# Performance work log

Measured on AMD Instinct MI355X. Metric: run time of the kernel, lower is better.

## Reference

```python
import jax, jax.numpy as jnp
import numpy as np

N_NODES = 100000
N_EDGES = 1600000
HIDDEN = 64
IN_CH = 6  # 3 (direction) + 3 (node feature part)
BN_EPS = 1e-5


def setup_inputs() -> dict:
    key = jax.random.key(0)
    ks = jax.random.split(key, 16)
    inp = {
        "x": jax.random.normal(ks[0], (N_NODES, 3), dtype=jnp.float32),
        "pos": jax.random.normal(ks[1], (N_NODES, 3), dtype=jnp.float32),
        "edge_index": jax.random.randint(ks[2], (2, N_EDGES), 0, N_NODES, dtype=jnp.int64),
    }
    dims = [IN_CH, HIDDEN, HIDDEN, HIDDEN]
    for i in range(3):
        din, dout = dims[i], dims[i + 1]
        inp[f"W{i+1}"] = jax.random.normal(ks[3 + 4 * i], (din, dout), dtype=jnp.float32) * (1.0 / np.sqrt(din))
        inp[f"b{i+1}"] = jnp.zeros((dout,), dtype=jnp.float32)
        inp[f"g{i+1}"] = jnp.ones((dout,), dtype=jnp.float32)   # BN gamma
        inp[f"be{i+1}"] = jnp.zeros((dout,), dtype=jnp.float32)  # BN beta
    return inp


def _mlp_layer(h, W, b, g, be):
    # Linear -> ReLU -> BatchNorm1d (training mode, biased variance like torch)
    h = jax.nn.relu(h @ W + b)
    mu = jnp.mean(h, axis=0)
    var = jnp.mean((h - mu) ** 2, axis=0)
    return g * (h - mu) * jax.lax.rsqrt(var + BN_EPS) + be


def reference(x, pos, edge_index, W1, b1, g1, be1, W2, b2, g2, be2, W3, b3, g3, be3):
    n = x.shape[0]
    xp = jnp.concatenate([pos, x], axis=1)             # [N, 3+F]
    src, dst = edge_index[0], edge_index[1]            # j = src, i = dst (PyG source_to_target)
    x_j = xp[src]                                      # [E, 3+F]
    x_i = xp[dst]
    direction = x_j[:, :3] - x_i[:, :3]                # [E, 3]
    # NOTE: source uses torch.norm with no dim => single global scalar norm
    direction = direction / jnp.linalg.norm(direction)
    h = jnp.concatenate([direction, x_i[:, 3:]], axis=-1)  # [E, IN_CH]
    h = _mlp_layer(h, W1, b1, g1, be1)
    h = _mlp_layer(h, W2, b2, g2, be2)
    h = _mlp_layer(h, W3, b3, g3, be3)                 # [E, HIDDEN]
    out = jax.ops.segment_max(h, dst, num_segments=n)  # scatter-max aggregation
    out = jnp.where(jnp.isfinite(out), out, 0.0)       # PyG fills empty segments with 0
    return out
```

## Files before the change

### kernel.cpp

```cpp
#include <hip/hip_runtime.h>
#include <stdint.h>

typedef unsigned short u16;
typedef unsigned int u32;
typedef __attribute__((ext_vector_type(8))) short short8;
typedef __attribute__((ext_vector_type(4))) float floatx4;

#define BN_EPS 1e-5f
#define NPB 64
#define NPB_SHIFT 6
#define NBMAX 2048

__device__ __forceinline__ float bf2f(u16 u) { return __uint_as_float(((unsigned)u) << 16); }
__device__ __forceinline__ u16 f2bf(float f) {
  unsigned u = __float_as_uint(f);
  u += 0x7FFFu + ((u >> 16) & 1u);
  return (u16)(u >> 16);
}
__device__ __forceinline__ u32 fkey(float f) {
  unsigned u = __float_as_uint(f);
  return (u >> 31) ? ~u : (u | 0x80000000u);
}
__device__ __forceinline__ float funkey(u32 k) {
  return (k & 0x80000000u) ? __uint_as_float(k ^ 0x80000000u) : __uint_as_float(~k);
}

__global__ void k_init(float* __restrict__ stats, u32* __restrict__ bucketTotal) {
  for (int i = threadIdx.x; i < 1024; i += blockDim.x) stats[i] = 0.f;
  for (int i = threadIdx.x; i < NBMAX + 1; i += blockDim.x) bucketTotal[i] = 0u;
}

__global__ void k_norm_hist(const int* __restrict__ ei, const float* __restrict__ pos,
                            int E, int NB, float* __restrict__ stats,
                            u32* __restrict__ bucketTotal) {
  __shared__ u32 lh[NBMAX];
  __shared__ float red[16];
  for (int i = threadIdx.x; i < NB; i += blockDim.x) lh[i] = 0u;
  __syncthreads();
  int tid = blockIdx.x * blockDim.x + threadIdx.x;
  int stride = gridDim.x * blockDim.x;
  float acc = 0.f;
  for (int e = tid; e < E; e += stride) {
    int s = ei[e], d = ei[E + e];
    float d0 = pos[3 * s + 0] - pos[3 * d + 0];
    float d1 = pos[3 * s + 1] - pos[3 * d + 1];
    float d2 = pos[3 * s + 2] - pos[3 * d + 2];
    acc = fmaf(d0, d0, acc);
    acc = fmaf(d1, d1, acc);
    acc = fmaf(d2, d2, acc);
    atomicAdd(&lh[d >> NPB_SHIFT], 1u);
  }
#pragma unroll
  for (int off = 32; off > 0; off >>= 1) acc += __shfl_down(acc, off, 64);
  if ((threadIdx.x & 63) == 0) red[threadIdx.x >> 6] = acc;
  __syncthreads();
  if (threadIdx.x == 0) {
    float s = 0.f;
    for (int w = 0; w < (int)(blockDim.x >> 6); w++) s += red[w];
    atomicAdd(&stats[0], s);
  }
  for (int i = threadIdx.x; i < NB; i += blockDim.x)
    if (lh[i]) atomicAdd(&bucketTotal[i], lh[i]);
}

__global__ void k_scan(const u32* __restrict__ bucketTotal, u32* __restrict__ base,
                       u32* __restrict__ cursor, int NB) {
  int lane = threadIdx.x;
  u32 run = 0;
  for (int b0 = 0; b0 < NB; b0 += 64) {
    int b = b0 + lane;
    u32 v = (b < NB) ? bucketTotal[b] : 0u;
    u32 s = v;
#pragma unroll
    for (int off = 1; off < 64; off <<= 1) {
      u32 t = __shfl_up(s, off, 64);
      if (lane >= off) s += t;
    }
    u32 excl = run + s - v;
    if (b < NB) { base[b] = excl; cursor[b] = excl; }
    run += __shfl(s, 63, 64);
  }
  if (lane == 0) base[NB] = run;
}

__global__ void k_place(const int* __restrict__ ei, int E, int NB,
                        u32* __restrict__ cursor, u32* __restrict__ sorted) {
  __shared__ u32 lh[NBMAX];
  __shared__ u32 lbase[NBMAX];
  for (int i = threadIdx.x; i < NB; i += blockDim.x) lh[i] = 0u;
  __syncthreads();
  int tid = blockIdx.x * blockDim.x + threadIdx.x;
  int stride = gridDim.x * blockDim.x;
  for (int e = tid; e < E; e += stride) atomicAdd(&lh[ei[E + e] >> NPB_SHIFT], 1u);
  __syncthreads();
  for (int i = threadIdx.x; i < NB; i += blockDim.x) {
    u32 c = lh[i];
    lbase[i] = c ? atomicAdd(&cursor[i], c) : 0u;
    lh[i] = 0u;
  }
  __syncthreads();
  for (int e = tid; e < E; e += stride) {
    int d = ei[E + e];
    int b = d >> NPB_SHIFT;
    u32 slot = lbase[b] + atomicAdd(&lh[b], 1u);
    sorted[slot] = ((u32)e << 8) | (u32)(d & (NPB - 1));
  }
}

__global__ __launch_bounds__(256) void k_bucket_max(
    const u32* __restrict__ sorted, const u32* __restrict__ base,
    const u16* __restrict__ h, const float* __restrict__ gsum3,
    const float* __restrict__ gsq3, const float* __restrict__ g3,
    const float* __restrict__ be3, float invE, float* __restrict__ outf, int N) {
  __shared__ u32 tile[NPB * 64];
  for (int i = threadIdx.x; i < NPB * 64; i += blockDim.x) tile[i] = 0u;
  int b = blockIdx.x;
  u32 start = base[b];
  int cnt = (int)(base[b + 1] - start);
  int t = threadIdx.x;
  int es = t >> 3;
  int c0 = (t & 7) * 8;
  float sc[8], sh[8];
#pragma unroll
  for (int j = 0; j < 8; j++) {
    int c = c0 + j;
    float mu = gsum3[c] * invE;
    float var = gsq3[c] * invE - mu * mu;
    float s = g3[c] * rsqrtf(var + BN_EPS);
    sc[j] = s;
    sh[j] = be3[c] - mu * s;
  }
  __syncthreads();

  const int SLOTS = 32;
  for (int i0 = 0; i0 < cnt; i0 += SLOTS * 4) {
    u32 pk[4];
    uint4 raw[4];
    int ok[4];
#pragma unroll
    for (int u_ = 0; u_ < 4; u_++) {
      int sl = i0 + u_ * SLOTS + es;
      ok[u_] = sl < cnt;
      pk[u_] = ok[u_] ? sorted[start + sl] : 0u;
    }
#pragma unroll
    for (int u_ = 0; u_ < 4; u_++)
      if (ok[u_]) raw[u_] = *(const uint4*)(h + (long)(pk[u_] >> 8) * 64 + c0);
#pragma unroll
    for (int u_ = 0; u_ < 4; u_++) {
      if (!ok[u_]) continue;
      int ln = (int)(pk[u_] & (u32)(NPB - 1));
      unsigned w[4] = {raw[u_].x, raw[u_].y, raw[u_].z, raw[u_].w};
      u32 key[8];
#pragma unroll
      for (int p = 0; p < 4; p++) {
        float v0 = bf2f((u16)(w[p] & 0xFFFFu));
        float v1 = bf2f((u16)(w[p] >> 16));
        key[2 * p] = fkey(fmaf(v0, sc[2 * p], sh[2 * p]));
        key[2 * p + 1] = fkey(fmaf(v1, sc[2 * p + 1], sh[2 * p + 1]));
      }
#pragma unroll
      for (int jj = 0; jj < 8; jj++) {
        int j = (jj + es) & 7;
        atomicMax(&tile[ln * 64 + c0 + j], key[j]);
      }
    }
  }
  __syncthreads();
  int node0 = b * NPB;
  for (int l = t; l < NPB * 64; l += blockDim.x) {
    int node = node0 + (l >> 6);
    if (node < N) {
      u32 k = tile[l];
      outf[(long)node * 64 + (l & 63)] = (k == 0u) ? 0.f : funkey(k);
    }
  }
}

__global__ __launch_bounds__(256) void k_layer1(
    const int* __restrict__ ei, const float* __restrict__ pos,
    const float* __restrict__ x, const float* __restrict__ W1,
    const float* __restrict__ b1, u16* __restrict__ h,
    const float* __restrict__ stats, float* __restrict__ gsum,
    float* __restrict__ gsq, int E) {
  __shared__ float in6[6][256];
  __shared__ float ssum[64], ssq[64];
  float invn = 1.0f / sqrtf(stats[0]);
  int t = threadIdx.x;
  int lane = t & 63;
  int wv = t >> 6;
  float w[6];
#pragma unroll
  for (int k = 0; k < 6; k++) w[k] = W1[k * 64 + lane];
  float bias = b1[lane];
  float psum = 0.f, psq = 0.f;

  int chunks = (E + 255) >> 8;
  for (int c = blockIdx.x; c < chunks; c += gridDim.x) {
    long e0 = (long)c << 8;
    int e = (int)e0 + t;
    float v[6] = {0.f, 0.f, 0.f, 0.f, 0.f, 0.f};
    if (e < E) {
      int s = ei[e], d = ei[E + e];
      float p0 = pos[3 * s + 0], p1 = pos[3 * s + 1], p2 = pos[3 * s + 2];
      float q0 = pos[3 * d + 0], q1 = pos[3 * d + 1], q2 = pos[3 * d + 2];
      v[0] = (p0 - q0) * invn;
      v[1] = (p1 - q1) * invn;
      v[2] = (p2 - q2) * invn;
      v[3] = x[3 * d + 0];
      v[4] = x[3 * d + 1];
      v[5] = x[3 * d + 2];
    }
    __syncthreads();
#pragma unroll
    for (int k = 0; k < 6; k++) in6[k][t] = v[k];
    __syncthreads();
    int lim = E - (int)e0;
    if (lim > 256) lim = 256;
    int base = wv * 64;
#pragma unroll 4
    for (int i = 0; i < 64; i++) {
      int el = base + i;
      if (el >= lim) break;
      float acc = bias;
#pragma unroll
      for (int k = 0; k < 6; k++) acc = fmaf(in6[k][el], w[k], acc);
      acc = fmaxf(acc, 0.f);
      u16 hb = f2bf(acc);
      h[(e0 + el) * 64 + lane] = hb;
      float hf = bf2f(hb);
      psum += hf;
      psq = fmaf(hf, hf, psq);
    }
  }
  if (t < 64) { ssum[t] = 0.f; ssq[t] = 0.f; }
  __syncthreads();
  atomicAdd(&ssum[lane], psum);
  atomicAdd(&ssq[lane], psq);
  __syncthreads();
  if (t < 64) {
    atomicAdd(&gsum[t], ssum[t]);
    atomicAdd(&gsq[t], ssq[t]);
  }
}

__global__ __launch_bounds__(256) void k_layer_mfma(
    u16* h, const float* __restrict__ W, const float* __restrict__ b,
    const float* __restrict__ gsum_in, const float* __restrict__ gsq_in,
    const float* __restrict__ g_in, const float* __restrict__ be_in, float invE,
    float* __restrict__ gsum, float* __restrict__ gsq, int E) {
  __shared__ float sc_s[64], sh_s[64];
  if (threadIdx.x < 64) {
    int c = threadIdx.x;
    float mu = gsum_in[c] * invE;
    float var = gsq_in[c] * invE - mu * mu;
    float s = g_in[c] * rsqrtf(var + BN_EPS);
    sc_s[c] = s;
    sh_s[c] = be_in[c] - mu * s;
  }
  __syncthreads();

  int lane = threadIdx.x & 63;
  int m = lane & 15;
  int q = lane >> 4;

  short8 bf[4][2];
  float bias[4];
#pragma unroll
  for (int t = 0; t < 4; t++) {
    int n = t * 16 + m;
    float bb = b[n];
    for (int k = 0; k < 64; k++) bb = fmaf(sh_s[k], W[k * 64 + n], bb);
    bias[t] = bb;
#pragma unroll
    for (int s = 0; s < 2; s++)
#pragma unroll
      for (int j = 0; j < 8; j++) {
        int k = s * 32 + q * 8 + j;
        bf[t][s][j] = (short)f2bf(W[k * 64 + n] * sc_s[k]);
      }
  }

  float psum[4] = {0.f, 0.f, 0.f, 0.f}, psq[4] = {0.f, 0.f, 0.f, 0.f};

  int tiles = E >> 4;
  int gw = ((int)blockIdx.x * (blockDim.x >> 6)) + (threadIdx.x >> 6);
  int nw = (int)gridDim.x * (blockDim.x >> 6);

  for (int tile = gw; tile < tiles; tile += nw) {
    long e0 = (long)tile * 16;
    const u16* rowp = h + (e0 + m) * 64 + q * 8;
    short8 a0 = *(const short8*)(rowp);
    short8 a1 = *(const short8*)(rowp + 32);
    floatx4 acc[4];
#pragma unroll
    for (int t = 0; t < 4; t++) acc[t] = (floatx4){0.f, 0.f, 0.f, 0.f};
#pragma unroll
    for (int t = 0; t < 4; t++)
      acc[t] = __builtin_amdgcn_mfma_f32_16x16x32_bf16(a0, bf[t][0], acc[t], 0, 0, 0);
#pragma unroll
    for (int t = 0; t < 4; t++)
      acc[t] = __builtin_amdgcn_mfma_f32_16x16x32_bf16(a1, bf[t][1], acc[t], 0, 0, 0);

#pragma unroll
    for (int t = 0; t < 4; t++) {
#pragma unroll
      for (int r = 0; r < 4; r++) {
        float v = acc[t][r] + bias[t];
        v = fmaxf(v, 0.f);
        u16 hb = f2bf(v);
        h[(e0 + q * 4 + r) * 64 + t * 16 + m] = hb;
        float hf = bf2f(hb);
        psum[t] += hf;
        psq[t] = fmaf(hf, hf, psq[t]);
      }
    }
  }

#pragma unroll
  for (int t = 0; t < 4; t++) {
    psum[t] += __shfl_xor(psum[t], 16, 64);
    psum[t] += __shfl_xor(psum[t], 32, 64);
    psq[t] += __shfl_xor(psq[t], 16, 64);
    psq[t] += __shfl_xor(psq[t], 32, 64);
  }
  __shared__ float ssum[64], ssq[64];
  if (threadIdx.x < 64) { ssum[threadIdx.x] = 0.f; ssq[threadIdx.x] = 0.f; }
  __syncthreads();
  if (q == 0) {
#pragma unroll
    for (int t = 0; t < 4; t++) {
      atomicAdd(&ssum[t * 16 + m], psum[t]);
      atomicAdd(&ssq[t * 16 + m], psq[t]);
    }
  }
  __syncthreads();
  if (threadIdx.x < 64) {
    atomicAdd(&gsum[threadIdx.x], ssum[threadIdx.x]);
    atomicAdd(&gsq[threadIdx.x], ssq[threadIdx.x]);
  }
}

__global__ void k_initout(float* __restrict__ outf, long n, float* __restrict__ stats,
                          u32* __restrict__ bucketTotal) {
  long i = (long)blockIdx.x * blockDim.x + threadIdx.x;
  long stride = (long)gridDim.x * blockDim.x;
  for (long j = i; j < n; j += stride) outf[j] = __uint_as_float(0xFF800000u);
  if (i < 1024) stats[i] = 0.f;
  if (i < NBMAX + 1) bucketTotal[i] = 0u;
}
__global__ void k_scatter(const int* __restrict__ ei, const u16* __restrict__ h,
                          const float* __restrict__ gsum3, const float* __restrict__ gsq3,
                          const float* __restrict__ g3, const float* __restrict__ be3,
                          float invE, float* outf, int E) {
  int lane = threadIdx.x & 63;
  int gw = ((int)blockIdx.x * (blockDim.x >> 6)) + (threadIdx.x >> 6);
  int nw = (int)gridDim.x * (blockDim.x >> 6);
  float mu = gsum3[lane] * invE;
  float var = gsq3[lane] * invE - mu * mu;
  float sc = g3[lane] * rsqrtf(var + BN_EPS);
  float sh = be3[lane] - mu * sc;
  for (int e = gw; e < E; e += nw) {
    int d = ei[E + e];
    float v = fmaf(bf2f(h[(long)e * 64 + lane]), sc, sh);
    float* addr = outf + (long)d * 64 + lane;
    if (v >= 0.f)
      atomicMax((int*)addr, __float_as_int(v));
    else
      atomicMin((unsigned int*)addr, __float_as_uint(v));
  }
}
__global__ void k_out(float* __restrict__ outf, long n) {
  long i = (long)blockIdx.x * blockDim.x + threadIdx.x;
  long stride = (long)gridDim.x * blockDim.x;
  for (long j = i; j < n; j += stride) {
    float v = outf[j];
    unsigned u = __float_as_uint(v);
    if ((u & 0x7F800000u) == 0x7F800000u) v = 0.f;
    outf[j] = v;
  }
}

extern "C" void kernel_launch(void* const* d_in, const int* in_sizes, int n_in,
                              void* d_out, int out_size, void* d_ws, size_t ws_size,
                              hipStream_t stream) {
  const float* x = (const float*)d_in[0];
  const float* pos = (const float*)d_in[1];
  const int* ei = (const int*)d_in[2];
  const float* W1 = (const float*)d_in[3];
  const float* b1 = (const float*)d_in[4];
  const float* g1 = (const float*)d_in[5];
  const float* be1 = (const float*)d_in[6];
  const float* W2 = (const float*)d_in[7];
  const float* b2 = (const float*)d_in[8];
  const float* g2 = (const float*)d_in[9];
  const float* be2 = (const float*)d_in[10];
  const float* W3 = (const float*)d_in[11];
  const float* b3 = (const float*)d_in[12];
  const float* g3 = (const float*)d_in[13];
  const float* be3 = (const float*)d_in[14];

  int N = in_sizes[0] / 3;
  int E = in_sizes[2] / 2;
  int NB = (N + NPB - 1) / NPB;
  long n_out = (long)N * 64;

  char* wsb = (char*)d_ws;
  u16* h = (u16*)wsb;
  size_t off = (size_t)E * 64 * 2;
  float* stats = (float*)(wsb + off);
  off += 1024 * 4;
  u32* bucketTotal = (u32*)(wsb + off);
  off += (NBMAX + 1) * 4;
  u32* baseArr = (u32*)(wsb + off);
  off += (NBMAX + 1) * 4;
  u32* cursor = (u32*)(wsb + off);
  off += NBMAX * 4;
  u32* sorted = (u32*)(wsb + off);
  off += (size_t)E * 4;
  size_t need = off;

  float* gsum1 = stats + 64, * gsq1 = stats + 128;
  float* gsum2 = stats + 192, * gsq2 = stats + 256;
  float* gsum3 = stats + 320, * gsq3 = stats + 384;

  float* outf = (float*)d_out;
  float invE = 1.0f / (float)E;
  bool binned = (ws_size >= need) && (NB <= NBMAX);

  if (binned) {
    k_init<<<1, 1024, 0, stream>>>(stats, bucketTotal);
    k_norm_hist<<<256, 256, 0, stream>>>(ei, pos, E, NB, stats, bucketTotal);
    k_scan<<<1, 64, 0, stream>>>(bucketTotal, baseArr, cursor, NB);
    k_place<<<256, 256, 0, stream>>>(ei, E, NB, cursor, sorted);
    k_layer1<<<1024, 256, 0, stream>>>(ei, pos, x, W1, b1, h, stats, gsum1, gsq1, E);
    k_layer_mfma<<<1024, 256, 0, stream>>>(h, W2, b2, gsum1, gsq1, g1, be1, invE, gsum2, gsq2, E);
    k_layer_mfma<<<1024, 256, 0, stream>>>(h, W3, b3, gsum2, gsq2, g2, be2, invE, gsum3, gsq3, E);
    k_bucket_max<<<NB, 256, 0, stream>>>(sorted, baseArr, h, gsum3, gsq3, g3, be3, invE, outf, N);
  } else {
    k_initout<<<4096, 256, 0, stream>>>(outf, n_out, stats, bucketTotal);
    k_norm_hist<<<256, 256, 0, stream>>>(ei, pos, E, NB <= NBMAX ? NB : 1, stats, bucketTotal);
    k_layer1<<<1024, 256, 0, stream>>>(ei, pos, x, W1, b1, h, stats, gsum1, gsq1, E);
    k_layer_mfma<<<1024, 256, 0, stream>>>(h, W2, b2, gsum1, gsq1, g1, be1, invE, gsum2, gsq2, E);
    k_layer_mfma<<<1024, 256, 0, stream>>>(h, W3, b3, gsum2, gsq2, g2, be2, invE, gsum3, gsq3, E);
    k_scatter<<<2048, 256, 0, stream>>>(ei, h, gsum3, gsq3, g3, be3, invE, outf, E);
    k_out<<<2048, 256, 0, stream>>>(outf, n_out);
  }
}
```

Before: 485.4 us.

## Process edges in bucket-sorted order and max over raw bf16 before BN

Layer 1 now reads edges through the bucket-sorted permutation, so the hidden activations h are stored in sorted order and the final bucket-max kernel reads them contiguously instead of gathering rows by edge id. The max reduction also works directly on bf16 bit patterns: keys are flipped per channel by the sign of gamma, and the affine BN transform is applied once per output element instead of once per edge element. This trades a scattered 128-byte row gather for streaming reads and removes per-edge float math. The risk is that layer 1 now does an extra indirection with scattered reads of the edge index. The bf16 key comparison also assumes nonnegative post-ReLU values and monotone ordering of the bit patterns.

Result: slower. 495.4 us (+2.1%).

```diff
diff --git a/kernel.cpp b/kernel.cpp
--- a/kernel.cpp
+++ b/kernel.cpp
@@ -16,13 +16,6 @@
   unsigned u = __float_as_uint(f);
   u += 0x7FFFu + ((u >> 16) & 1u);
   return (u16)(u >> 16);
-}
-__device__ __forceinline__ u32 fkey(float f) {
-  unsigned u = __float_as_uint(f);
-  return (u >> 31) ? ~u : (u | 0x80000000u);
-}
-__device__ __forceinline__ float funkey(u32 k) {
-  return (k & 0x80000000u) ? __uint_as_float(k ^ 0x80000000u) : __uint_as_float(~k);
 }
 
 __global__ void k_init(float* __restrict__ stats, u32* __restrict__ bucketTotal) {
@@ -120,59 +113,61 @@
   int t = threadIdx.x;
   int es = t >> 3;
   int c0 = (t & 7) * 8;
-  float sc[8], sh[8];
-#pragma unroll
-  for (int j = 0; j < 8; j++) {
-    int c = c0 + j;
-    float mu = gsum3[c] * invE;
-    float var = gsq3[c] * invE - mu * mu;
-    float s = g3[c] * rsqrtf(var + BN_EPS);
-    sc[j] = s;
-    sh[j] = be3[c] - mu * s;
-  }
-  __syncthreads();
-
-  const int SLOTS = 32;
-  for (int i0 = 0; i0 < cnt; i0 += SLOTS * 4) {
-    u32 pk[4];
+  u32 mm[4];
+#pragma unroll
+  for (int p = 0; p < 4; p++) {
+    u32 m0 = (g3[c0 + 2 * p] < 0.f) ? 0xFFFFu : 0u;
+    u32 m1 = (g3[c0 + 2 * p + 1] < 0.f) ? 0xFFFFu : 0u;
+    mm[p] = m0 | (m1 << 16);
+  }
+  __syncthreads();
+
+  for (int i0 = 0; i0 < cnt; i0 += 128) {
     uint4 raw[4];
+    u32 ln[4];
     int ok[4];
 #pragma unroll
     for (int u_ = 0; u_ < 4; u_++) {
-      int sl = i0 + u_ * SLOTS + es;
+      int sl = i0 + u_ * 32 + es;
       ok[u_] = sl < cnt;
-      pk[u_] = ok[u_] ? sorted[start + sl] : 0u;
-    }
-#pragma unroll
-    for (int u_ = 0; u_ < 4; u_++)
-      if (ok[u_]) raw[u_] = *(const uint4*)(h + (long)(pk[u_] >> 8) * 64 + c0);
+      if (ok[u_]) {
+        ln[u_] = sorted[start + sl] & (u32)(NPB - 1);
+        raw[u_] = *(const uint4*)(h + (long)(start + sl) * 64 + c0);
+      }
+    }
 #pragma unroll
     for (int u_ = 0; u_ < 4; u_++) {
       if (!ok[u_]) continue;
-      int ln = (int)(pk[u_] & (u32)(NPB - 1));
       unsigned w[4] = {raw[u_].x, raw[u_].y, raw[u_].z, raw[u_].w};
       u32 key[8];
 #pragma unroll
       for (int p = 0; p < 4; p++) {
-        float v0 = bf2f((u16)(w[p] & 0xFFFFu));
-        float v1 = bf2f((u16)(w[p] >> 16));
-        key[2 * p] = fkey(fmaf(v0, sc[2 * p], sh[2 * p]));
-        key[2 * p + 1] = fkey(fmaf(v1, sc[2 * p + 1], sh[2 * p + 1]));
+        u32 wx = w[p] ^ mm[p];
+        key[2 * p] = (wx & 0xFFFFu) | 0x10000u;
+        key[2 * p + 1] = (wx >> 16) | 0x10000u;
       }
+      u32 baseA = ln[u_] * 64u + (u32)c0;
 #pragma unroll
       for (int jj = 0; jj < 8; jj++) {
         int j = (jj + es) & 7;
-        atomicMax(&tile[ln * 64 + c0 + j], key[j]);
+        atomicMax(&tile[baseA + j], key[j]);
       }
     }
   }
   __syncthreads();
+  int c = t & 63;
+  float mu = gsum3[c] * invE;
+  float var = gsq3[c] * invE - mu * mu;
+  float sc = g3[c] * rsqrtf(var + BN_EPS);
+  float sh = be3[c] - mu * sc;
+  u32 me = (g3[c] < 0.f) ? 0xFFFFu : 0u;
   int node0 = b * NPB;
   for (int l = t; l < NPB * 64; l += blockDim.x) {
     int node = node0 + (l >> 6);
     if (node < N) {
       u32 k = tile[l];
-      outf[(long)node * 64 + (l & 63)] = (k == 0u) ? 0.f : funkey(k);
+      float v = (k == 0u) ? 0.f : fmaf(bf2f((u16)((k & 0xFFFFu) ^ me)), sc, sh);
+      outf[(long)node * 64 + (l & 63)] = v;
     }
   }
 }
@@ -182,7 +177,7 @@
     const float* __restrict__ x, const float* __restrict__ W1,
     const float* __restrict__ b1, u16* __restrict__ h,
     const float* __restrict__ stats, float* __restrict__ gsum,
-    float* __restrict__ gsq, int E) {
+    float* __restrict__ gsq, int E, const u32* __restrict__ sorted) {
   __shared__ float in6[6][256];
   __shared__ float ssum[64], ssq[64];
   float invn = 1.0f / sqrtf(stats[0]);
@@ -201,7 +196,8 @@
     int e = (int)e0 + t;
     float v[6] = {0.f, 0.f, 0.f, 0.f, 0.f, 0.f};
     if (e < E) {
-      int s = ei[e], d = ei[E + e];
+      int eid = sorted ? (int)(sorted[e] >> 8) : e;
+      int s = ei[eid], d = ei[E + eid];
       float p0 = pos[3 * s + 0], p1 = pos[3 * s + 1], p2 = pos[3 * s + 2];
       float q0 = pos[3 * d + 0], q1 = pos[3 * d + 1], q2 = pos[3 * d + 2];
       v[0] = (p0 - q0) * invn;
@@ -433,14 +429,14 @@
     k_norm_hist<<<256, 256, 0, stream>>>(ei, pos, E, NB, stats, bucketTotal);
     k_scan<<<1, 64, 0, stream>>>(bucketTotal, baseArr, cursor, NB);
     k_place<<<256, 256, 0, stream>>>(ei, E, NB, cursor, sorted);
-    k_layer1<<<1024, 256, 0, stream>>>(ei, pos, x, W1, b1, h, stats, gsum1, gsq1, E);
+    k_layer1<<<1024, 256, 0, stream>>>(ei, pos, x, W1, b1, h, stats, gsum1, gsq1, E, sorted);
     k_layer_mfma<<<1024, 256, 0, stream>>>(h, W2, b2, gsum1, gsq1, g1, be1, invE, gsum2, gsq2, E);
     k_layer_mfma<<<1024, 256, 0, stream>>>(h, W3, b3, gsum2, gsq2, g2, be2, invE, gsum3, gsq3, E);
     k_bucket_max<<<NB, 256, 0, stream>>>(sorted, baseArr, h, gsum3, gsq3, g3, be3, invE, outf, N);
   } else {
     k_initout<<<4096, 256, 0, stream>>>(outf, n_out, stats, bucketTotal);
     k_norm_hist<<<256, 256, 0, stream>>>(ei, pos, E, NB <= NBMAX ? NB : 1, stats, bucketTotal);
-    k_layer1<<<1024, 256, 0, stream>>>(ei, pos, x, W1, b1, h, stats, gsum1, gsq1, E);
+    k_layer1<<<1024, 256, 0, stream>>>(ei, pos, x, W1, b1, h, stats, gsum1, gsq1, E, (const u32*)nullptr);
     k_layer_mfma<<<1024, 256, 0, stream>>>(h, W2, b2, gsum1, gsq1, g1, be1, invE, gsum2, gsq2, E);
     k_layer_mfma<<<1024, 256, 0, stream>>>(h, W3, b3, gsum2, gsq2, g2, be2, invE, gsum3, gsq3, E);
     k_scatter<<<2048, 256, 0, stream>>>(ei, h, gsum3, gsq3, g3, be3, invE, outf, E);
```
